# Performance work log

Hardware: AMD Instinct MI355X
Metric: run time of the kernel (lower is better)

The kernel has to match this reference:

```python
import jax, jax.numpy as jnp
import numpy as np

VOCAB, EMB, H, D3, CTX = 30522, 768, 1024, 128, 512

def setup_inputs() -> dict:
    key = jax.random.key(0)
    ks = jax.random.split(key, 12)
    B, S = 8, 64
    inp = {
        'decoder_input_ids': jax.random.randint(ks[0], (B, S), 0, VOCAB, dtype=jnp.int64) if jax.config.jax_enable_x64 else jax.random.randint(ks[0], (B, S), 0, VOCAB, dtype=jnp.int32),
        'decoder_attn_mask': jnp.ones((B, S), dtype=jnp.int32),
        'decoder_seq_type_id': jnp.zeros((B, S), dtype=jnp.int32),
        'h_first': jax.random.normal(ks[1], (B, H), dtype=jnp.float32),
        'context': jax.random.normal(ks[2], (B, CTX, H), dtype=jnp.float32),
        # learned parameters (torch Linear stored transposed as [in, out])
        'emb_table': jax.random.normal(ks[3], (VOCAB, EMB), dtype=jnp.float32) * 0.02,
        'W_in': jax.random.normal(ks[4], (EMB, H), dtype=jnp.float32) * 0.02,
        'b_in': jnp.zeros((H,), dtype=jnp.float32),
        'W_s': jax.random.normal(ks[5], (H, H), dtype=jnp.float32) * 0.02,
        'b_s': jnp.zeros((H,), dtype=jnp.float32),
        'W_att_in': jax.random.normal(ks[6], (2 * H, D3), dtype=jnp.float32) * 0.02,
        'b_att_in': jnp.zeros((D3,), dtype=jnp.float32),
        'W_att_h': jax.random.normal(ks[7], (H, D3), dtype=jnp.float32) * 0.02,
        'b_att_h': jnp.zeros((D3,), dtype=jnp.float32),
        'V': jax.random.uniform(ks[8], (D3,), dtype=jnp.float32, minval=-1.0, maxval=1.0),
    }
    return inp


def reference(decoder_input_ids, decoder_attn_mask, decoder_seq_type_id, h_first,
              context, emb_table, W_in, b_in, W_s, b_s,
              W_att_in, b_att_in, W_att_h, b_att_h, V):
    # bert_embedding stub: plain token embedding lookup -> [B, S, 768]
    feats = emb_table[decoder_input_ids]
    # hidden_dense(context) is constant across steps; hoist it (same math)
    ctx_proj = context @ W_att_h + b_att_h          # [B, ctx, d3]
    h0 = context[:, -1, :]                          # initial recurrent state
    xs = jnp.swapaxes(feats, 0, 1)                  # [S, B, 768]

    def step(h, t_i):
        h = h @ W_s + b_s                           # dense_s
        s = jnp.concatenate([t_i @ W_in + b_in, h], axis=1)   # [B, 2H]
        a = jnp.tanh((s @ W_att_in + b_att_in)[:, None, :] + ctx_proj)  # [B,ctx,d3]
        att_before = jnp.einsum('d,bcd->bc', V, a)  # bmm(v, a^T) squeezed -> [B, ctx]
        # faithful to original: softmax over dim=1 of [B,1,ctx] (size-1 axis -> all ones)
        att_after = jax.nn.softmax(att_before[:, None, :], axis=1)[:, 0, :]
        idx = jnp.argmax(att_after, axis=1)         # ties -> 0, matches torch .max(1)
        return h, (att_before, idx)

    _, (atts, prts) = jax.lax.scan(step, h0, xs)
    atts = jnp.swapaxes(atts, 0, 1)                 # stack(dim=1).squeeze() -> [B, S, ctx]
    return atts, prts
```

## Files before the change

kernel.cpp:

```cpp
#include <hip/hip_runtime.h>
#include <hip/hip_bf16.h>

#define EMB 768
#define HD 1024
#define D3 128
#define CTXN 512
#define BB 8
#define SS 64

typedef __attribute__((ext_vector_type(8))) short short8v;
typedef __attribute__((ext_vector_type(4))) float f32x4;

__device__ __forceinline__ float fast_tanh(float x) {
  float e = __expf(2.f * x);
  return 1.f - 2.f * __builtin_amdgcn_rcpf(e + 1.f);
}
__device__ __forceinline__ float bf2f(__hip_bfloat16 x) { return __bfloat162float(x); }

struct GDesc {
  const void* A;
  const __hip_bfloat16* BT;
  const int* arowmap;
  const float* addrow_f;
  const float* bias_f;
  float* Cf;
  __hip_bfloat16* Cb;
  __hip_bfloat16* CbT;
  float* brow_f;
  int M, N, K, lda, ldbt, ldct, af32, mtiles, blk0, nblks;
};
struct GBatch { GDesc d[10]; int nd; };

__global__ __launch_bounds__(256) void gemmz(GBatch bat) {
  int bx = blockIdx.x;
  GDesc d = bat.d[0];
  for (int i = 1; i < bat.nd; ++i)
    if (bx >= bat.d[i].blk0) d = bat.d[i];
  int local = bx - d.blk0;
  int mt = local % d.mtiles, nt = local / d.mtiles;
  int bm0 = mt * 32, bn0 = nt * 64;

  __shared__ __hip_bfloat16 As[2][32][128];
  __shared__ __hip_bfloat16 Bs[2][64][128];
  int tid = threadIdx.x, lane = tid & 63, wid = tid >> 6;
  int l16 = lane & 15, g = lane >> 4;
  int wm = (wid & 1) * 16, wn = (wid >> 1) * 32;
  int arow = tid >> 3, aseg = tid & 7;
  int brow = tid >> 2, bseg = tid & 3;
  f32x4 acc[2] = {};

  int agr = bm0 + arow;
  int asrc = (agr < d.M) ? (d.arowmap ? d.arowmap[agr] : agr) : -1;
  const float* Af = (const float*)d.A;
  const __hip_bfloat16* Ab = (const __hip_bfloat16*)d.A;

  float fa[16];
  short8v ba0 = {}, ba1 = {}, bb0 = {}, bb1 = {}, bb2 = {}, bb3 = {};
  int nk = d.K >> 7;

  auto LD = [&](int k0) {
    if (d.af32) {
      if (asrc >= 0) {
        const float* s = Af + (long)asrc * d.lda + k0 + aseg * 16;
#pragma unroll
        for (int j = 0; j < 16; ++j) fa[j] = s[j];
      } else {
#pragma unroll
        for (int j = 0; j < 16; ++j) fa[j] = 0.f;
      }
    } else {
      if (asrc >= 0) {
        const __hip_bfloat16* s = Ab + (long)asrc * d.lda + k0 + aseg * 16;
        ba0 = *(const short8v*)s;
        ba1 = *(const short8v*)(s + 8);
      } else {
        short8v z = {};
        ba0 = z; ba1 = z;
      }
    }
    const __hip_bfloat16* bsrc = d.BT + (long)(bn0 + brow) * d.ldbt + k0 + bseg * 32;
    bb0 = *(const short8v*)bsrc;
    bb1 = *(const short8v*)(bsrc + 8);
    bb2 = *(const short8v*)(bsrc + 16);
    bb3 = *(const short8v*)(bsrc + 24);
  };
  auto ST = [&](int buf) {
    int rs = arow & 7;
    if (d.af32) {
      __hip_bfloat16 t8[16];
#pragma unroll
      for (int j = 0; j < 16; ++j) t8[j] = __float2bfloat16(fa[j]);
      *(short8v*)&As[buf][arow][((2 * aseg) ^ rs) * 8] = *(short8v*)t8;
      *(short8v*)&As[buf][arow][((2 * aseg + 1) ^ rs) * 8] = *(short8v*)(t8 + 8);
    } else {
      *(short8v*)&As[buf][arow][((2 * aseg) ^ rs) * 8] = ba0;
      *(short8v*)&As[buf][arow][((2 * aseg + 1) ^ rs) * 8] = ba1;
    }
    int rb = brow & 7;
    *(short8v*)&Bs[buf][brow][((4 * bseg) ^ rb) * 8] = bb0;
    *(short8v*)&Bs[buf][brow][((4 * bseg + 1) ^ rb) * 8] = bb1;
    *(short8v*)&Bs[buf][brow][((4 * bseg + 2) ^ rb) * 8] = bb2;
    *(short8v*)&Bs[buf][brow][((4 * bseg + 3) ^ rb) * 8] = bb3;
  };

  LD(0);
  ST(0);
  __syncthreads();
  for (int it = 0; it < nk; ++it) {
    int cur = it & 1;
    if (it + 1 < nk) LD((it + 1) << 7);
    int ar = wm + l16;
    int ars = ar & 7;
#pragma unroll
    for (int kf = 0; kf < 4; ++kf) {
      short8v a = *(const short8v*)&As[cur][ar][((kf * 4 + g) ^ ars) * 8];
#pragma unroll
      for (int j = 0; j < 2; ++j) {
        int br = wn + j * 16 + l16;
        short8v b = *(const short8v*)&Bs[cur][br][((kf * 4 + g) ^ (br & 7)) * 8];
        acc[j] = __builtin_amdgcn_mfma_f32_16x16x32_bf16(a, b, acc[j], 0, 0, 0);
      }
    }
    if (it + 1 < nk) ST(cur ^ 1);
    __syncthreads();
  }

  float* Cs = (float*)&Bs[0][0][0];
  bool doT = (d.CbT != nullptr);
#pragma unroll
  for (int j = 0; j < 2; ++j)
#pragma unroll
    for (int r = 0; r < 4; ++r) {
      int gl = wm + g * 4 + r, cl = wn + j * 16 + l16;
      int grow = bm0 + gl, gcol = bn0 + cl;
      float v = acc[j][r];
      if (d.bias_f) v += d.bias_f[gcol];
      if (d.addrow_f && grow == d.M - 1) v += d.addrow_f[gcol];
      if (grow < d.M) {
        if (d.Cf) d.Cf[(long)grow * d.N + gcol] = v;
        if (d.Cb) d.Cb[(long)grow * d.N + gcol] = __float2bfloat16(v);
        if (d.brow_f && grow == d.M - 1) d.brow_f[gcol] = v;
      }
      if (doT) Cs[cl * 33 + gl] = v;
    }
  if (doT) {
    __syncthreads();
    int ctrows = d.M < 1024 ? d.M : 1024;
    int n = tid >> 2, ms = (tid & 3) * 8;
    int gm0 = bm0 + ms;
    __hip_bfloat16 t8[8];
#pragma unroll
    for (int jj = 0; jj < 8; ++jj) t8[jj] = __float2bfloat16(Cs[n * 33 + ms + jj]);
    if (gm0 + 7 < ctrows) {
      *(short8v*)&d.CbT[(long)(bn0 + n) * d.ldct + gm0] = *(short8v*)t8;
    } else {
#pragma unroll
      for (int jj = 0; jj < 8; ++jj)
        if (gm0 + jj < ctrows) d.CbT[(long)(bn0 + n) * d.ldct + gm0 + jj] = t8[jj];
    }
  }
}

__global__ __launch_bounds__(256) void kcast(const float* __restrict__ W_s,
                                             const float* __restrict__ b_s,
                                             const float* __restrict__ context,
                                             const float* __restrict__ b_in,
                                             const float* __restrict__ W_att_in,
                                             const float* __restrict__ b_att_in,
                                             const float* __restrict__ W_att_h,
                                             const int* __restrict__ ids,
                                             __hip_bfloat16* __restrict__ Mb0,
                                             __hip_bfloat16* __restrict__ Mb0T,
                                             __hip_bfloat16* __restrict__ Y0T,
                                             __hip_bfloat16* __restrict__ WahT,
                                             __hip_bfloat16* __restrict__ WaiT,
                                             __hip_bfloat16* __restrict__ Gb,
                                             float* __restrict__ qb,
                                             int* __restrict__ rowmap) {
  int blk = blockIdx.x, tid = threadIdx.x;
  __shared__ __hip_bfloat16 tl[64][65];
  __shared__ float red[2][128];

  auto TP = [&](const float* src, int R, int C, __hip_bfloat16* dst, int tr, int tc) {
    int r0 = tr * 64, c0 = tc * 64;
    {
      int r = tid >> 2, cs = (tid & 3) * 16;
      const float* s = src + (long)(r0 + r) * C + c0 + cs;
#pragma unroll
      for (int j = 0; j < 16; ++j) tl[cs + j][r] = __float2bfloat16(s[j]);
    }
    __syncthreads();
    {
      int c = tid >> 2, rs = (tid & 3) * 16;
      __hip_bfloat16 o[16];
#pragma unroll
      for (int j = 0; j < 16; ++j) o[j] = tl[c][rs + j];
      *(short8v*)&dst[(long)(c0 + c) * R + r0 + rs] = *(short8v*)&o[0];
      *(short8v*)&dst[(long)(c0 + c) * R + r0 + rs + 8] = *(short8v*)&o[8];
    }
  };

  if (blk < 256) {
    long base = (long)blk * 4096;
    for (int i = tid; i < 4096; i += 256)
      Mb0[base + i] = __float2bfloat16(W_s[base + i]);
  } else if (blk == 256) {
    for (int i = tid; i < HD; i += 256)
      Mb0[(long)HD * HD + i] = __float2bfloat16(b_s[i]);
  } else if (blk < 513) {
    int t = blk - 257;
    TP(W_s, 1024, 1024, Mb0T, t >> 4, t & 15);
  } else if (blk < 545) {
    int t = blk - 513;
    TP(W_att_in + (long)1024 * D3, 1024, 128, Y0T, t >> 1, t & 1);
  } else if (blk < 577) {
    int t = blk - 545;
    TP(W_att_h, 1024, 128, WahT, t >> 1, t & 1);
  } else if (blk < 609) {
    int t = blk - 577;
    TP(W_att_in, 1024, 128, WaiT, t >> 1, t & 1);
  } else if (blk == 609) {
    for (int i = tid; i < BB * HD; i += 256) {
      int b = i >> 10, k = i & 1023;
      Gb[i] = __float2bfloat16(context[((long)b * CTXN + CTXN - 1) * HD + k]);
    }
  } else if (blk == 610) {
    int dd = tid & 127, h = tid >> 7;
    float acc = 0.f;
    for (int k = h * 512; k < h * 512 + 512; ++k)
      acc += b_in[k] * W_att_in[k * D3 + dd];
    red[h][dd] = acc;
    __syncthreads();
    if (h == 0) qb[dd] = red[0][dd] + red[1][dd] + b_att_in[dd];
  } else {
    for (int i = tid; i < 512; i += 256) {
      int t = i >> 3, b = i & 7;
      rowmap[i] = ids[b * SS + t];
    }
  }
}

__global__ __launch_bounds__(256) void katt(const float* __restrict__ qF,
                                            const float* __restrict__ qH,
                                            const float* __restrict__ ctxp,
                                            const float* __restrict__ V,
                                            float* __restrict__ out) {
  int blk = blockIdx.x;
  int b = blk >> 5, tt = (blk >> 4) & 1, ct = blk & 15;
  int t0 = tt * 32, c0 = ct * 32;
  int tid = threadIdx.x;
  __shared__ float lq[32][128];
  __shared__ float lc[32][132];
  __shared__ float lv[128];
  for (int i = tid; i < 32 * 128; i += 256) {
    int r = i >> 7, d = i & 127;
    int t = t0 + r;
    lq[r][d] = qF[((long)t * 8 + b) * 128 + d] +
               qH[(((long)(t & 7)) * 64 + (t >> 3) * 8 + b) * 128 + d];
    lc[r][d] = ctxp[((long)b * CTXN + c0 + r) * D3 + d];
  }
  if (tid < 128) lv[tid] = V[tid];
  __syncthreads();
  int cl = tid & 31, tg = tid >> 5;
  float r[4] = {0.f, 0.f, 0.f, 0.f};
  for (int d4 = 0; d4 < 32; ++d4) {
    float4 cv = *reinterpret_cast<const float4*>(&lc[cl][d4 * 4]);
    float4 vv = *reinterpret_cast<const float4*>(&lv[d4 * 4]);
#pragma unroll
    for (int u = 0; u < 4; ++u) {
      int t = tg + u * 8;
      float4 qv = *reinterpret_cast<const float4*>(&lq[t][d4 * 4]);
      r[u] = fmaf(vv.x, fast_tanh(qv.x + cv.x), r[u]);
      r[u] = fmaf(vv.y, fast_tanh(qv.y + cv.y), r[u]);
      r[u] = fmaf(vv.z, fast_tanh(qv.z + cv.z), r[u]);
      r[u] = fmaf(vv.w, fast_tanh(qv.w + cv.w), r[u]);
    }
  }
#pragma unroll
  for (int u = 0; u < 4; ++u) {
    int t = tg + u * 8;
    out[((long)b * SS + (t0 + t)) * CTXN + c0 + cl] = r[u];
  }
  if (blk == 0) {
    for (int i = tid; i < SS * BB; i += 256) out[(long)BB * SS * CTXN + i] = 0.f;
  }
}

static inline GDesc mk(const void* A, int af32, int lda, const int* arowmap,
                       const __hip_bfloat16* BT, int ldbt, int M, int N, int K,
                       const float* addrow_f, const float* bias_f, float* Cf,
                       __hip_bfloat16* Cb, __hip_bfloat16* CbT, int ldct,
                       float* brow_f, int blk0) {
  GDesc d;
  d.A = A; d.BT = BT; d.arowmap = arowmap;
  d.addrow_f = addrow_f; d.bias_f = bias_f;
  d.Cf = Cf; d.Cb = Cb; d.CbT = CbT; d.brow_f = brow_f;
  d.M = M; d.N = N; d.K = K; d.lda = lda; d.ldbt = ldbt; d.ldct = ldct;
  d.af32 = af32;
  d.mtiles = (M + 31) >> 5;
  d.blk0 = blk0;
  d.nblks = d.mtiles * (N >> 6);
  return d;
}

extern "C" void kernel_launch(void* const* d_in, const int* in_sizes, int n_in,
                              void* d_out, int out_size, void* d_ws, size_t ws_size,
                              hipStream_t stream) {
  const int* ids = (const int*)d_in[0];
  const float* context = (const float*)d_in[4];
  const float* emb = (const float*)d_in[5];
  const float* W_in = (const float*)d_in[6];
  const float* b_in = (const float*)d_in[7];
  const float* W_s = (const float*)d_in[8];
  const float* b_s = (const float*)d_in[9];
  const float* W_att_in = (const float*)d_in[10];
  const float* b_att_in = (const float*)d_in[11];
  const float* W_att_h = (const float*)d_in[12];
  const float* b_att_h = (const float*)d_in[13];
  const float* V = (const float*)d_in[14];

  float* ws = (float*)d_ws;
  float* ctxp = ws;
  float* Yf = ctxp + 524288;
  float* qF = Yf + 1180800;
  float* qH = qF + 65536;
  float* qb = qH + 65536;
  float* brow2 = qb + 128;
  float* brow4 = brow2 + 1024;
  float* brow8 = brow4 + 1024;
  float* brow16 = brow8 + 1024;
  float* brow32 = brow16 + 1024;
  int* rowmap = (int*)(brow32 + 1024);
  __hip_bfloat16* bfp = (__hip_bfloat16*)(rowmap + 512);
  __hip_bfloat16* Mb0 = bfp;
  __hip_bfloat16* Mb0T = Mb0 + 1049600;
  __hip_bfloat16* Mb1 = Mb0T + 1048576;
  __hip_bfloat16* Mb1T = Mb1 + 1049600;
  __hip_bfloat16* Mb2 = Mb1T + 1048576;
  __hip_bfloat16* Mb2T = Mb2 + 1049600;
  __hip_bfloat16* Mb3 = Mb2T + 1048576;
  __hip_bfloat16* Mb3T = Mb3 + 1049600;
  __hip_bfloat16* YT = Mb3T + 1048576;
  __hip_bfloat16* WahT = YT + 9 * 131072;
  __hip_bfloat16* WaiT = WahT + 131072;
  __hip_bfloat16* WcT = WaiT + 131072;
  __hip_bfloat16* Gb = WcT + 131072;
  float* out = (float*)d_out;

  auto Yfr = [&](int r) { return Yf + (long)r * 131200; };
  auto YTs = [&](int r) { return YT + (long)r * 131072; };

  kcast<<<dim3(612), dim3(256), 0, stream>>>(W_s, b_s, context, b_in, W_att_in,
                                             b_att_in, W_att_h, ids, Mb0, Mb0T,
                                             YTs(0), WahT, WaiT, Gb, qb, rowmap);
  {
    GBatch bt{}; int c = 0;
    bt.d[0] = mk(Mb0, 0, 1024, nullptr, Mb0T, 1024, 1025, 1024, 1024, b_s, nullptr, nullptr, Mb1, Mb1T, 1024, brow2, c); c += bt.d[0].nblks;
    bt.d[1] = mk(Mb0, 0, 1024, nullptr, YTs(0), 1024, 1025, 128, 1024, nullptr, nullptr, Yfr(1), nullptr, YTs(1), 1024, nullptr, c); c += bt.d[1].nblks;
    bt.d[2] = mk(context, 1, 1024, nullptr, WahT, 1024, 4096, 128, 1024, nullptr, b_att_h, ctxp, nullptr, nullptr, 0, nullptr, c); c += bt.d[2].nblks;
    bt.d[3] = mk(W_in, 1, 1024, nullptr, WaiT, 1024, 768, 128, 1024, nullptr, nullptr, nullptr, nullptr, WcT, 768, nullptr, c); c += bt.d[3].nblks;
    bt.nd = 4;
    gemmz<<<dim3(c), dim3(256), 0, stream>>>(bt);
  }
  {
    GBatch bt{}; int c = 0;
    bt.d[0] = mk(Mb1, 0, 1024, nullptr, Mb1T, 1024, 1025, 1024, 1024, brow2, nullptr, nullptr, Mb2, Mb2T, 1024, brow4, c); c += bt.d[0].nblks;
    bt.d[1] = mk(Mb1, 0, 1024, nullptr, YTs(0), 1024, 1025, 128, 1024, nullptr, nullptr, Yfr(2), nullptr, YTs(2), 1024, nullptr, c); c += bt.d[1].nblks;
    bt.d[2] = mk(Mb1, 0, 1024, nullptr, YTs(1), 1024, 1025, 128, 1024, Yfr(1) + 131072, nullptr, Yfr(3), nullptr, YTs(3), 1024, nullptr, c); c += bt.d[2].nblks;
    bt.nd = 3;
    gemmz<<<dim3(c), dim3(256), 0, stream>>>(bt);
  }
  {
    GBatch bt{}; int c = 0;
    bt.d[0] = mk(Mb2, 0, 1024, nullptr, Mb2T, 1024, 1025, 1024, 1024, brow4, nullptr, nullptr, Mb3, Mb3T, 1024, brow8, c); c += bt.d[0].nblks;
    for (int s = 0; s < 4; ++s) {
      bt.d[1 + s] = mk(Mb2, 0, 1024, nullptr, YTs(s), 1024, 1025, 128, 1024,
                       (s == 0) ? nullptr : (Yfr(s) + 131072), nullptr,
                       Yfr(4 + s), nullptr, YTs(4 + s), 1024, nullptr, c);
      c += bt.d[1 + s].nblks;
    }
    bt.nd = 5;
    gemmz<<<dim3(c), dim3(256), 0, stream>>>(bt);
  }
  {
    GBatch bt{}; int c = 0;
    bt.d[0] = mk(Mb3, 0, 1024, nullptr, Mb3T, 1024, 1025, 1024, 1024, brow8, nullptr, nullptr, Mb1, Mb1T, 1024, brow16, c); c += bt.d[0].nblks;
    bt.d[1] = mk(Mb3, 0, 1024, nullptr, YTs(0), 1024, 1025, 128, 1024, nullptr, nullptr, Yfr(8), nullptr, YTs(8), 1024, nullptr, c); c += bt.d[1].nblks;
    bt.d[2] = mk(Gb, 0, 1024, nullptr, Mb3T, 1024, 8, 1024, 1024, nullptr, brow8, nullptr, Gb + 8192, nullptr, 0, nullptr, c); c += bt.d[2].nblks;
    bt.nd = 3;
    gemmz<<<dim3(c), dim3(256), 0, stream>>>(bt);
  }
  {
    GBatch bt{}; int c = 0;
    bt.d[0] = mk(Mb1, 0, 1024, nullptr, Mb1T, 1024, 1025, 1024, 1024, brow16, nullptr, nullptr, Mb2, Mb2T, 1024, brow32, c); c += bt.d[0].nblks;
    bt.d[1] = mk(Gb, 0, 1024, nullptr, Mb1T, 1024, 16, 1024, 1024, nullptr, brow16, nullptr, Gb + 16384, nullptr, 0, nullptr, c); c += bt.d[1].nblks;
    bt.nd = 2;
    gemmz<<<dim3(c), dim3(256), 0, stream>>>(bt);
  }
  {
    GBatch bt{}; int c = 0;
    bt.d[0] = mk(Gb, 0, 1024, nullptr, Mb2T, 1024, 32, 1024, 1024, nullptr, brow32, nullptr, Gb + 32768, nullptr, 0, nullptr, c); c += bt.d[0].nblks;
    bt.nd = 1;
    gemmz<<<dim3(c), dim3(256), 0, stream>>>(bt);
  }
  {
    GBatch bt{}; int c = 0;
    for (int r = 1; r <= 8; ++r) {
      bt.d[r - 1] = mk(Gb, 0, 1024, nullptr, YTs(r), 1024, 64, 128, 1024, nullptr,
                       Yfr(r) + 131072, qH + (long)(r - 1) * 8192, nullptr, nullptr,
                       0, nullptr, c);
      c += bt.d[r - 1].nblks;
    }
    bt.d[8] = mk(emb, 1, 768, rowmap, WcT, 768, 512, 128, 768, nullptr, qb, qF,
                 nullptr, nullptr, 0, nullptr, c);
    c += bt.d[8].nblks;
    bt.nd = 9;
    gemmz<<<dim3(c), dim3(256), 0, stream>>>(bt);
  }
  katt<<<dim3(256), dim3(256), 0, stream>>>(qF, qH, ctxp, V, out);
}
```

Baseline: 151.9 us.

## Pre-cast context to bf16, remap blocks across XCDs, move embedding GEMM earlier

Adds 1024 extra kcast blocks that convert the full context tensor to bf16, so the large context projection GEMM reads bf16 instead of converting fp32 in its load path. Remaps block indices so that consecutive logical tiles land on the same XCD, which is meant to improve L2 locality on MI355X. Moves the embedding-feature GEMM from the last batched launch into the second one to shorten the critical-path tail. This costs an extra full pass over context (read fp32, write bf16) and some extra memory.

```diff
diff --git a/kernel.cpp b/kernel.cpp
--- a/kernel.cpp
+++ b/kernel.cpp
@@ -8,6 +8,7 @@
 #define BB 8
 #define SS 64
 
+typedef __hip_bfloat16 bf16;
 typedef __attribute__((ext_vector_type(8))) short short8v;
 typedef __attribute__((ext_vector_type(4))) float f32x4;
 
@@ -15,24 +16,27 @@
   float e = __expf(2.f * x);
   return 1.f - 2.f * __builtin_amdgcn_rcpf(e + 1.f);
 }
-__device__ __forceinline__ float bf2f(__hip_bfloat16 x) { return __bfloat162float(x); }
 
 struct GDesc {
   const void* A;
-  const __hip_bfloat16* BT;
+  const bf16* BT;
   const int* arowmap;
   const float* addrow_f;
   const float* bias_f;
   float* Cf;
-  __hip_bfloat16* Cb;
-  __hip_bfloat16* CbT;
+  bf16* Cb;
+  bf16* CbT;
   float* brow_f;
   int M, N, K, lda, ldbt, ldct, af32, mtiles, blk0, nblks;
 };
 struct GBatch { GDesc d[10]; int nd; };
 
 __global__ __launch_bounds__(256) void gemmz(GBatch bat) {
-  int bx = blockIdx.x;
+  int nwg = gridDim.x, orig = blockIdx.x;
+  int q8 = nwg >> 3, r8 = nwg & 7;
+  int xcd = orig & 7, idx = orig >> 3;
+  int bx = (xcd < r8 ? xcd * (q8 + 1) : r8 * (q8 + 1) + (xcd - r8) * q8) + idx;
+
   GDesc d = bat.d[0];
   for (int i = 1; i < bat.nd; ++i)
     if (bx >= bat.d[i].blk0) d = bat.d[i];
@@ -40,8 +44,8 @@
   int mt = local % d.mtiles, nt = local / d.mtiles;
   int bm0 = mt * 32, bn0 = nt * 64;
 
-  __shared__ __hip_bfloat16 As[2][32][128];
-  __shared__ __hip_bfloat16 Bs[2][64][128];
+  __shared__ bf16 As[2][32][128];
+  __shared__ bf16 Bs[2][64][128];
   int tid = threadIdx.x, lane = tid & 63, wid = tid >> 6;
   int l16 = lane & 15, g = lane >> 4;
   int wm = (wid & 1) * 16, wn = (wid >> 1) * 32;
@@ -52,7 +56,7 @@
   int agr = bm0 + arow;
   int asrc = (agr < d.M) ? (d.arowmap ? d.arowmap[agr] : agr) : -1;
   const float* Af = (const float*)d.A;
-  const __hip_bfloat16* Ab = (const __hip_bfloat16*)d.A;
+  const bf16* Ab = (const bf16*)d.A;
 
   float fa[16];
   short8v ba0 = {}, ba1 = {}, bb0 = {}, bb1 = {}, bb2 = {}, bb3 = {};
@@ -70,7 +74,7 @@
       }
     } else {
       if (asrc >= 0) {
-        const __hip_bfloat16* s = Ab + (long)asrc * d.lda + k0 + aseg * 16;
+        const bf16* s = Ab + (long)asrc * d.lda + k0 + aseg * 16;
         ba0 = *(const short8v*)s;
         ba1 = *(const short8v*)(s + 8);
       } else {
@@ -78,7 +82,7 @@
         ba0 = z; ba1 = z;
       }
     }
-    const __hip_bfloat16* bsrc = d.BT + (long)(bn0 + brow) * d.ldbt + k0 + bseg * 32;
+    const bf16* bsrc = d.BT + (long)(bn0 + brow) * d.ldbt + k0 + bseg * 32;
     bb0 = *(const short8v*)bsrc;
     bb1 = *(const short8v*)(bsrc + 8);
     bb2 = *(const short8v*)(bsrc + 16);
@@ -87,7 +91,7 @@
   auto ST = [&](int buf) {
     int rs = arow & 7;
     if (d.af32) {
-      __hip_bfloat16 t8[16];
+      bf16 t8[16];
 #pragma unroll
       for (int j = 0; j < 16; ++j) t8[j] = __float2bfloat16(fa[j]);
       *(short8v*)&As[buf][arow][((2 * aseg) ^ rs) * 8] = *(short8v*)t8;
@@ -148,7 +152,7 @@
     int ctrows = d.M < 1024 ? d.M : 1024;
     int n = tid >> 2, ms = (tid & 3) * 8;
     int gm0 = bm0 + ms;
-    __hip_bfloat16 t8[8];
+    bf16 t8[8];
 #pragma unroll
     for (int jj = 0; jj < 8; ++jj) t8[jj] = __float2bfloat16(Cs[n * 33 + ms + jj]);
     if (gm0 + 7 < ctrows) {
@@ -169,19 +173,20 @@
                                              const float* __restrict__ b_att_in,
                                              const float* __restrict__ W_att_h,
                                              const int* __restrict__ ids,
-                                             __hip_bfloat16* __restrict__ Mb0,
-                                             __hip_bfloat16* __restrict__ Mb0T,
-                                             __hip_bfloat16* __restrict__ Y0T,
-                                             __hip_bfloat16* __restrict__ WahT,
-                                             __hip_bfloat16* __restrict__ WaiT,
-                                             __hip_bfloat16* __restrict__ Gb,
+                                             bf16* __restrict__ Mb0,
+                                             bf16* __restrict__ Mb0T,
+                                             bf16* __restrict__ Y0T,
+                                             bf16* __restrict__ WahT,
+                                             bf16* __restrict__ WaiT,
+                                             bf16* __restrict__ Gb,
                                              float* __restrict__ qb,
-                                             int* __restrict__ rowmap) {
+                                             int* __restrict__ rowmap,
+                                             bf16* __restrict__ ctxb) {
   int blk = blockIdx.x, tid = threadIdx.x;
-  __shared__ __hip_bfloat16 tl[64][65];
+  __shared__ bf16 tl[64][65];
   __shared__ float red[2][128];
 
-  auto TP = [&](const float* src, int R, int C, __hip_bfloat16* dst, int tr, int tc) {
+  auto TP = [&](const float* src, int R, int C, bf16* dst, int tr, int tc) {
     int r0 = tr * 64, c0 = tc * 64;
     {
       int r = tid >> 2, cs = (tid & 3) * 16;
@@ -192,7 +197,7 @@
     __syncthreads();
     {
       int c = tid >> 2, rs = (tid & 3) * 16;
-      __hip_bfloat16 o[16];
+      bf16 o[16];
 #pragma unroll
       for (int j = 0; j < 16; ++j) o[j] = tl[c][rs + j];
       *(short8v*)&dst[(long)(c0 + c) * R + r0 + rs] = *(short8v*)&o[0];
@@ -232,11 +237,27 @@
     red[h][dd] = acc;
     __syncthreads();
     if (h == 0) qb[dd] = red[0][dd] + red[1][dd] + b_att_in[dd];
-  } else {
+  } else if (blk == 611) {
     for (int i = tid; i < 512; i += 256) {
       int t = i >> 3, b = i & 7;
       rowmap[i] = ids[b * SS + t];
     }
+  } else {
+    long base = (long)(blk - 612) * 4096;
+    const float4* src = (const float4*)(context + base);
+    int f0 = tid * 4;
+    float4 v0 = src[f0], v1 = src[f0 + 1], v2 = src[f0 + 2], v3 = src[f0 + 3];
+    bf16 o[16];
+    o[0] = __float2bfloat16(v0.x); o[1] = __float2bfloat16(v0.y);
+    o[2] = __float2bfloat16(v0.z); o[3] = __float2bfloat16(v0.w);
+    o[4] = __float2bfloat16(v1.x); o[5] = __float2bfloat16(v1.y);
+    o[6] = __float2bfloat16(v1.z); o[7] = __float2bfloat16(v1.w);
+    o[8] = __float2bfloat16(v2.x); o[9] = __float2bfloat16(v2.y);
+    o[10] = __float2bfloat16(v2.z); o[11] = __float2bfloat16(v2.w);
+    o[12] = __float2bfloat16(v3.x); o[13] = __float2bfloat16(v3.y);
+    o[14] = __float2bfloat16(v3.z); o[15] = __float2bfloat16(v3.w);
+    *(short8v*)&ctxb[base + tid * 16] = *(short8v*)&o[0];
+    *(short8v*)&ctxb[base + tid * 16 + 8] = *(short8v*)&o[8];
   }
 }
 
@@ -262,7 +283,7 @@
   if (tid < 128) lv[tid] = V[tid];
   __syncthreads();
   int cl = tid & 31, tg = tid >> 5;
-  float r[4] = {0.f, 0.f, 0.f, 0.f};
+  float r4[4] = {0.f, 0.f, 0.f, 0.f};
   for (int d4 = 0; d4 < 32; ++d4) {
     float4 cv = *reinterpret_cast<const float4*>(&lc[cl][d4 * 4]);
     float4 vv = *reinterpret_cast<const float4*>(&lv[d4 * 4]);
@@ -270,16 +291,16 @@
     for (int u = 0; u < 4; ++u) {
       int t = tg + u * 8;
       float4 qv = *reinterpret_cast<const float4*>(&lq[t][d4 * 4]);
-      r[u] = fmaf(vv.x, fast_tanh(qv.x + cv.x), r[u]);
-      r[u] = fmaf(vv.y, fast_tanh(qv.y + cv.y), r[u]);
-      r[u] = fmaf(vv.z, fast_tanh(qv.z + cv.z), r[u]);
-      r[u] = fmaf(vv.w, fast_tanh(qv.w + cv.w), r[u]);
+      r4[u] = fmaf(vv.x, fast_tanh(qv.x + cv.x), r4[u]);
+      r4[u] = fmaf(vv.y, fast_tanh(qv.y + cv.y), r4[u]);
+      r4[u] = fmaf(vv.z, fast_tanh(qv.z + cv.z), r4[u]);
+      r4[u] = fmaf(vv.w, fast_tanh(qv.w + cv.w), r4[u]);
     }
   }
 #pragma unroll
   for (int u = 0; u < 4; ++u) {
     int t = tg + u * 8;
-    out[((long)b * SS + (t0 + t)) * CTXN + c0 + cl] = r[u];
+    out[((long)b * SS + (t0 + t)) * CTXN + c0 + cl] = r4[u];
   }
   if (blk == 0) {
     for (int i = tid; i < SS * BB; i += 256) out[(long)BB * SS * CTXN + i] = 0.f;
@@ -287,10 +308,9 @@
 }
 
 static inline GDesc mk(const void* A, int af32, int lda, const int* arowmap,
-                       const __hip_bfloat16* BT, int ldbt, int M, int N, int K,
+                       const bf16* BT, int ldbt, int M, int N, int K,
                        const float* addrow_f, const float* bias_f, float* Cf,
-                       __hip_bfloat16* Cb, __hip_bfloat16* CbT, int ldct,
-                       float* brow_f, int blk0) {
+                       bf16* Cb, bf16* CbT, int ldct, float* brow_f, int blk0) {
   GDesc d;
   d.A = A; d.BT = BT; d.arowmap = arowmap;
   d.addrow_f = addrow_f; d.bias_f = bias_f;
@@ -331,33 +351,35 @@
   float* brow16 = brow8 + 1024;
   float* brow32 = brow16 + 1024;
   int* rowmap = (int*)(brow32 + 1024);
-  __hip_bfloat16* bfp = (__hip_bfloat16*)(rowmap + 512);
-  __hip_bfloat16* Mb0 = bfp;
-  __hip_bfloat16* Mb0T = Mb0 + 1049600;
-  __hip_bfloat16* Mb1 = Mb0T + 1048576;
-  __hip_bfloat16* Mb1T = Mb1 + 1049600;
-  __hip_bfloat16* Mb2 = Mb1T + 1048576;
-  __hip_bfloat16* Mb2T = Mb2 + 1049600;
-  __hip_bfloat16* Mb3 = Mb2T + 1048576;
-  __hip_bfloat16* Mb3T = Mb3 + 1049600;
-  __hip_bfloat16* YT = Mb3T + 1048576;
-  __hip_bfloat16* WahT = YT + 9 * 131072;
-  __hip_bfloat16* WaiT = WahT + 131072;
-  __hip_bfloat16* WcT = WaiT + 131072;
-  __hip_bfloat16* Gb = WcT + 131072;
+  bf16* bfp = (bf16*)(rowmap + 512);
+  bf16* Mb0 = bfp;
+  bf16* Mb0T = Mb0 + 1049600;
+  bf16* Mb1 = Mb0T + 1048576;
+  bf16* Mb1T = Mb1 + 1049600;
+  bf16* Mb2 = Mb1T + 1048576;
+  bf16* Mb2T = Mb2 + 1049600;
+  bf16* Mb3 = Mb2T + 1048576;
+  bf16* Mb3T = Mb3 + 1049600;
+  bf16* YT = Mb3T + 1048576;
+  bf16* WahT = YT + 9 * 131072;
+  bf16* WaiT = WahT + 131072;
+  bf16* WcT = WaiT + 131072;
+  bf16* Gb = WcT + 131072;
+  bf16* ctxb = Gb + 65536;
   float* out = (float*)d_out;
 
   auto Yfr = [&](int r) { return Yf + (long)r * 131200; };
   auto YTs = [&](int r) { return YT + (long)r * 131072; };
 
-  kcast<<<dim3(612), dim3(256), 0, stream>>>(W_s, b_s, context, b_in, W_att_in,
-                                             b_att_in, W_att_h, ids, Mb0, Mb0T,
-                                             YTs(0), WahT, WaiT, Gb, qb, rowmap);
+  kcast<<<dim3(1636), dim3(256), 0, stream>>>(W_s, b_s, context, b_in, W_att_in,
+                                              b_att_in, W_att_h, ids, Mb0, Mb0T,
+                                              YTs(0), WahT, WaiT, Gb, qb, rowmap,
+                                              ctxb);
   {
     GBatch bt{}; int c = 0;
     bt.d[0] = mk(Mb0, 0, 1024, nullptr, Mb0T, 1024, 1025, 1024, 1024, b_s, nullptr, nullptr, Mb1, Mb1T, 1024, brow2, c); c += bt.d[0].nblks;
     bt.d[1] = mk(Mb0, 0, 1024, nullptr, YTs(0), 1024, 1025, 128, 1024, nullptr, nullptr, Yfr(1), nullptr, YTs(1), 1024, nullptr, c); c += bt.d[1].nblks;
-    bt.d[2] = mk(context, 1, 1024, nullptr, WahT, 1024, 4096, 128, 1024, nullptr, b_att_h, ctxp, nullptr, nullptr, 0, nullptr, c); c += bt.d[2].nblks;
+    bt.d[2] = mk(ctxb, 0, 1024, nullptr, WahT, 1024, 4096, 128, 1024, nullptr, b_att_h, ctxp, nullptr, nullptr, 0, nullptr, c); c += bt.d[2].nblks;
     bt.d[3] = mk(W_in, 1, 1024, nullptr, WaiT, 1024, 768, 128, 1024, nullptr, nullptr, nullptr, nullptr, WcT, 768, nullptr, c); c += bt.d[3].nblks;
     bt.nd = 4;
     gemmz<<<dim3(c), dim3(256), 0, stream>>>(bt);
@@ -367,7 +389,8 @@
     bt.d[0] = mk(Mb1, 0, 1024, nullptr, Mb1T, 1024, 1025, 1024, 1024, brow2, nullptr, nullptr, Mb2, Mb2T, 1024, brow4, c); c += bt.d[0].nblks;
     bt.d[1] = mk(Mb1, 0, 1024, nullptr, YTs(0), 1024, 1025, 128, 1024, nullptr, nullptr, Yfr(2), nullptr, YTs(2), 1024, nullptr, c); c += bt.d[1].nblks;
     bt.d[2] = mk(Mb1, 0, 1024, nullptr, YTs(1), 1024, 1025, 128, 1024, Yfr(1) + 131072, nullptr, Yfr(3), nullptr, YTs(3), 1024, nullptr, c); c += bt.d[2].nblks;
-    bt.nd = 3;
+    bt.d[3] = mk(emb, 1, 768, rowmap, WcT, 768, 512, 128, 768, nullptr, qb, qF, nullptr, nullptr, 0, nullptr, c); c += bt.d[3].nblks;
+    bt.nd = 4;
     gemmz<<<dim3(c), dim3(256), 0, stream>>>(bt);
   }
   {
@@ -411,10 +434,7 @@
                        0, nullptr, c);
       c += bt.d[r - 1].nblks;
     }
-    bt.d[8] = mk(emb, 1, 768, rowmap, WcT, 768, 512, 128, 768, nullptr, qb, qF,
-                 nullptr, nullptr, 0, nullptr, c);
-    c += bt.d[8].nblks;
-    bt.nd = 9;
+    bt.nd = 8;
     gemmz<<<dim3(c), dim3(256), 0, stream>>>(bt);
   }
   katt<<<dim3(256), dim3(256), 0, stream>>>(qF, qH, ctxp, V, out);
```

After: 156.8 us. 3.2% more time.
